# Optimization experiments

Measured on AMD Instinct MI355X. Metric: run time of the kernel, lower is better.

## Reference

```python
import jax, jax.numpy as jnp
import numpy as np

N_LAYERS = 4
EPS = 1e-5  # eqx.nn.LayerNorm default


def _kernels(lam, P, B, C, step, L):
    # Annotated-S4 DPLR generating-function kernel (Q = P), vectorized over H channels.
    # lam, P, B, C: (H, N) complex64; step: (H, 1) real. Returns K: (H, L) real.
    omega = jnp.exp((-2j * jnp.pi) * (jnp.arange(L) / L))            # (L,) roots of unity
    g = (2.0 / step) * ((1.0 - omega) / (1.0 + omega))[None, :]      # (H, L) bilinear warp
    c = 2.0 / (1.0 + omega)                                          # (L,)

    def cauchy(v):  # v: (H, N) -> (H, L): sum_n v_n / (g - lambda_n)
        return jnp.sum(v[:, None, :] / (g[:, :, None] - lam[:, None, :]), axis=-1)

    k00 = cauchy(jnp.conj(C) * B)
    k01 = cauchy(jnp.conj(C) * P)
    k10 = cauchy(jnp.conj(P) * B)
    k11 = cauchy(jnp.conj(P) * P)
    at_roots = c[None, :] * (k00 - k01 * (1.0 / (1.0 + k11)) * k10)  # woodbury correction
    return jnp.fft.ifft(at_roots, n=L, axis=-1).real                 # (H, L)


def _causal_conv(u, K):
    # u: (B, L, H) real input, K: (H, L) real kernel -> causal conv along L via zero-padded FFT.
    L = u.shape[1]
    Ud = jnp.fft.rfft(u, n=2 * L, axis=1)                 # (B, F, H)
    Kd = jnp.fft.rfft(K, n=2 * L, axis=-1)                # (H, F)
    return jnp.fft.irfft(Ud * Kd.T[None], n=2 * L, axis=1)[:, :L]


def _forward(x, enc_w, enc_b, dec_w, dec_b, lam_re, lam_im, p_re, p_im, b_re, b_im,
             c_re, c_im, d, log_step, norm_w, norm_b, w1, b1, w2, b2):
    L = x.shape[1]
    h = x @ enc_w.T + enc_b                               # encoder: (B, L, H)
    for i in range(N_LAYERS):
        skip = h
        mu = h.mean(-1, keepdims=True)
        var = ((h - mu) ** 2).mean(-1, keepdims=True)
        hn = (h - mu) / jnp.sqrt(var + EPS) * norm_w[i] + norm_b[i]
        K = _kernels(lam_re[i] + 1j * lam_im[i], p_re[i] + 1j * p_im[i],
                     b_re[i] + 1j * b_im[i], c_re[i] + 1j * c_im[i],
                     jnp.exp(log_step[i])[:, None], L)
        y = _causal_conv(hn, K) + hn * d[i]               # SSM conv + skip-through D term
        y = jax.nn.gelu(y)
        y = (y @ w1[i].T + b1[i]) * jax.nn.sigmoid(y @ w2[i].T + b2[i])  # gated MLP
        h = skip + y
    return h @ dec_w.T + dec_b                            # decoder: (B, L, out)


def setup_inputs() -> dict:
    key = jax.random.key(0)
    B, L, IN, OUT, H, N, NL = 8, 2048, 64, 64, 128, 64, N_LAYERS
    ks = jax.random.split(key, 12)
    rn = lambda k, s, sc: (jax.random.normal(k, s) * sc).astype(jnp.float32)
    return dict(
        x=rn(ks[0], (B, L, IN), 1.0),
        convolve=1,
        enc_w=rn(ks[1], (H, IN), 1.0 / np.sqrt(IN)), enc_b=jnp.zeros((H,), jnp.float32),
        dec_w=rn(ks[2], (OUT, H), 1.0 / np.sqrt(H)), dec_b=jnp.zeros((OUT,), jnp.float32),
        lam_re=-0.5 * jnp.ones((NL, H, N), jnp.float32),  # HiPPO/S4D-style stable poles
        lam_im=jnp.tile(jnp.float32(np.pi) * jnp.arange(N, dtype=jnp.float32), (NL, H, 1)),
        p_re=rn(ks[3], (NL, H, N), 0.5 / np.sqrt(N)), p_im=rn(ks[4], (NL, H, N), 0.5 / np.sqrt(N)),
        b_re=rn(ks[5], (NL, H, N), 1.0), b_im=rn(ks[6], (NL, H, N), 1.0),
        c_re=rn(ks[7], (NL, H, N), 1.0 / np.sqrt(N)), c_im=rn(ks[8], (NL, H, N), 1.0 / np.sqrt(N)),
        d=jnp.ones((NL, H), jnp.float32),
        log_step=(jax.random.uniform(ks[9], (NL, H)) * (np.log(0.1) - np.log(0.001))
                  + np.log(0.001)).astype(jnp.float32),
        norm_w=jnp.ones((NL, H), jnp.float32), norm_b=jnp.zeros((NL, H), jnp.float32),
        w1=rn(ks[10], (NL, H, H), 1.0 / np.sqrt(H)), b1=jnp.zeros((NL, H), jnp.float32),
        w2=rn(ks[11], (NL, H, H), 1.0 / np.sqrt(H)), b2=jnp.zeros((NL, H), jnp.float32),
    )


def reference(x, convolve, enc_w, enc_b, dec_w, dec_b, lam_re, lam_im, p_re, p_im,
              b_re, b_im, c_re, c_im, d, log_step, norm_w, norm_b, w1, b1, w2, b2):
    # convolve is static 1 (True): the FFT-convolution path of the S4 Model.
    return _forward(x, enc_w, enc_b, dec_w, dec_b, lam_re, lam_im, p_re, p_im, b_re, b_im,
                    c_re, c_im, d, log_step, norm_w, norm_b, w1, b1, w2, b2)
```

## Files before the change

kernel.cpp:

```cpp
#include <hip/hip_runtime.h>
#include <hip/hip_bf16.h>


#define Bsz 8
#define Lseq 2048
#define Hdim 128
#define Npol 64
#define NLAYERS 4

typedef __bf16 bf16x8 __attribute__((ext_vector_type(8)));
typedef float f32x16 __attribute__((ext_vector_type(16)));

__device__ __forceinline__ float fast_rcp(float x) { return __builtin_amdgcn_rcpf(x); }
__device__ __forceinline__ float fast_rsq(float x) { return __builtin_amdgcn_rsqf(x); }

__device__ __forceinline__ float2 cmulf(float2 a, float2 b) {
    return make_float2(a.x * b.x - a.y * b.y, a.x * b.y + a.y * b.x);
}
__device__ __forceinline__ float2 cmulc(float2 a, float2 b) {
    return make_float2(a.x * b.x + a.y * b.y, a.y * b.x - a.x * b.y);
}

__device__ __forceinline__ float gelu_f(float v) {
    float z = 0.7978845608028654f * (v + 0.044715f * v * v * v);
    float e = __expf(2.0f * z);
    return v - v * fast_rcp(e + 1.0f);
}

__device__ __forceinline__ int sw(int i) { return (i & ~15) | ((i ^ (i >> 4)) & 15); }

static __device__ const float W16R[8] = {1.f, 0.9238795325f, 0.7071067812f, 0.3826834324f,
                                         0.f, -0.3826834324f, -0.7071067812f, -0.9238795325f};
static __device__ const float W16I[8] = {0.f, -0.3826834324f, -0.7071067812f, -0.9238795325f,
                                         -1.f, -0.9238795325f, -0.7071067812f, -0.3826834324f};
static __device__ const int BR4[16] = {0, 8, 4, 12, 2, 10, 6, 14, 1, 9, 5, 13, 3, 11, 7, 15};
static __device__ const int BR3[8] = {0, 4, 2, 6, 1, 5, 3, 7};

__device__ __forceinline__ float2 twget(const float2* __restrict__ tw, int e) {
    float2 w = tw[e & 2047];
    if (e & 2048) { w.x = -w.x; w.y = -w.y; }
    return w;
}

template <bool INV>
__device__ __forceinline__ void fft16_dif(float2 v[16]) {
#pragma unroll
    for (int mi = 0; mi < 4; mi++) {
        const int m = 8 >> mi;
#pragma unroll
        for (int g = 0; g < 16; g += 2 * m) {
#pragma unroll
            for (int j = 0; j < m; j++) {
                float wr = W16R[j << mi];
                float wi = INV ? -W16I[j << mi] : W16I[j << mi];
                float2 a = v[g + j], b = v[g + j + m];
                float dx = a.x - b.x, dy = a.y - b.y;
                v[g + j] = make_float2(a.x + b.x, a.y + b.y);
                v[g + j + m] = make_float2(dx * wr - dy * wi, dx * wi + dy * wr);
            }
        }
    }
}

template <bool INV>
__device__ __forceinline__ void fft16_dit(float2 v[16]) {
#pragma unroll
    for (int mi = 3; mi >= 0; mi--) {
        const int m = 8 >> mi;
#pragma unroll
        for (int g = 0; g < 16; g += 2 * m) {
#pragma unroll
            for (int j = 0; j < m; j++) {
                float wr = W16R[j << mi];
                float wi = INV ? -W16I[j << mi] : W16I[j << mi];
                float2 a = v[g + j], b = v[g + j + m];
                float bx = b.x * wr - b.y * wi, by = b.x * wi + b.y * wr;
                v[g + j] = make_float2(a.x + bx, a.y + by);
                v[g + j + m] = make_float2(a.x - bx, a.y - by);
            }
        }
    }
}

template <bool INV>
__device__ __forceinline__ void fft8_dif(float2 v[8]) {
#pragma unroll
    for (int mi = 0; mi < 3; mi++) {
        const int m = 4 >> mi;
#pragma unroll
        for (int g = 0; g < 8; g += 2 * m) {
#pragma unroll
            for (int j = 0; j < m; j++) {
                float wr = W16R[j << (mi + 1)];
                float wi = INV ? -W16I[j << (mi + 1)] : W16I[j << (mi + 1)];
                float2 a = v[g + j], b = v[g + j + m];
                float dx = a.x - b.x, dy = a.y - b.y;
                v[g + j] = make_float2(a.x + b.x, a.y + b.y);
                v[g + j + m] = make_float2(dx * wr - dy * wi, dx * wi + dy * wr);
            }
        }
    }
}

__device__ __forceinline__ void fft4096_passA_hz(float2* data, const float2* __restrict__ tw,
                                                 int t, const float2 vin[8]) {
    float2 v[16];
#pragma unroll
    for (int j = 0; j < 8; j++) v[j] = vin[j];
#pragma unroll
    for (int j = 0; j < 8; j++)
        v[j + 8] = cmulf(v[j], make_float2(W16R[j], W16I[j]));
#pragma unroll
    for (int mi = 1; mi < 4; mi++) {
        const int m = 8 >> mi;
#pragma unroll
        for (int g = 0; g < 16; g += 2 * m) {
#pragma unroll
            for (int j = 0; j < m; j++) {
                float wr = W16R[j << mi], wi = W16I[j << mi];
                float2 a = v[g + j], b = v[g + j + m];
                float dx = a.x - b.x, dy = a.y - b.y;
                v[g + j] = make_float2(a.x + b.x, a.y + b.y);
                v[g + j + m] = make_float2(dx * wr - dy * wi, dx * wi + dy * wr);
            }
        }
    }
#pragma unroll
    for (int i = 1; i < 16; i++) v[i] = cmulf(v[i], twget(tw, t * BR4[i]));
#pragma unroll
    for (int i = 0; i < 16; i++) data[sw(i * 256 + t)] = v[i];
}

__device__ __forceinline__ void fft4096_fwd_BC(float2* data, const float2* __restrict__ tw, int t) {
    __syncthreads();
    {
        int j0 = t & 15;
        int base = (t >> 4) * 256 + j0;
        float2 v[16];
#pragma unroll
        for (int k = 0; k < 16; k++) v[k] = data[sw(base + 16 * k)];
        fft16_dif<false>(v);
#pragma unroll
        for (int i = 1; i < 16; i++) v[i] = cmulf(v[i], twget(tw, 16 * j0 * BR4[i]));
#pragma unroll
        for (int i = 0; i < 16; i++) data[sw(base + 16 * i)] = v[i];
    }
    __syncthreads();
    {
        float2 v[16];
#pragma unroll
        for (int k = 0; k < 16; k++) v[k] = data[sw(t * 16 + k)];
        fft16_dif<false>(v);
#pragma unroll
        for (int i = 0; i < 16; i++) data[sw(t * 16 + i)] = v[i];
    }
    __syncthreads();
}

__global__ __launch_bounds__(256, 4) void prep_kernel(const float* __restrict__ lam_re,
                                                      const float* __restrict__ lam_im,
                                                      const float* __restrict__ p_re,
                                                      const float* __restrict__ p_im,
                                                      const float* __restrict__ b_re,
                                                      const float* __restrict__ b_im,
                                                      const float* __restrict__ c_re,
                                                      const float* __restrict__ c_im,
                                                      const float* __restrict__ log_step,
                                                      const float* __restrict__ w1,
                                                      const float* __restrict__ w2,
                                                      float2* __restrict__ tw,
                                                      __bf16* __restrict__ wbf,
                                                      float2* __restrict__ at_roots) {
    int bid = blockIdx.x, t = threadIdx.x;
    if (bid < 8) {
        int k = bid * 256 + t;
        if (k < 2048) {
            double a = -6.283185307179586476925286766559 * (double)k / 4096.0;
            tw[k] = make_float2((float)cos(a), (float)sin(a));
        }
        return;
    }
    if (bid < 264) {
        int i = (bid - 8) * 256 + t;
        int layer = i >> 14, rem = i & 16383;
        wbf[((size_t)layer * 2) * 16384 + rem] = (__bf16)w1[i];
        wbf[((size_t)layer * 2 + 1) * 16384 + rem] = (__bf16)w2[i];
        return;
    }
    int s = bid - 264;
    int h = s & 127, layer = (s >> 7) & 3;
    int l0 = 512 * (s >> 9);
    __shared__ __align__(16) float4 polA[Npol];
    __shared__ __align__(16) float4 polB[Npol];
    __shared__ float n11S[Npol];
    int baseP = (layer * Hdim + h) * Npol;
    if (t < Npol) {
        int n = t;
        float lr = lam_re[baseP + n], li = lam_im[baseP + n];
        float pr = p_re[baseP + n], pi = p_im[baseP + n];
        float br = b_re[baseP + n], bi = b_im[baseP + n];
        float cr = c_re[baseP + n], ci = c_im[baseP + n];
        polA[n] = make_float4(lr, li, cr * br + ci * bi, cr * bi - ci * br);
        polB[n] = make_float4(cr * pr + ci * pi, cr * pi - ci * pr,
                              pr * br + pi * bi, pr * bi - pi * br);
        n11S[n] = pr * pr + pi * pi;
    }
    __syncthreads();
    float step = expf(log_step[layer * Hdim + h]);
    float gs = 2.0f / step;

    float gr[2], gi[2];
#pragma unroll
    for (int j = 0; j < 2; j++) {
        int l = l0 + t + 256 * j;
        float ang = -6.283185307179586f * (float)l / (float)Lseq;
        float wr = cosf(ang), wi = sinf(ang);
        float dr = 1.0f + wr, di = wi;
        float invd2 = fast_rcp(dr * dr + di * di);
        float nr = 1.0f - wr, ni = -wi;
        gr[j] = gs * (nr * dr + ni * di) * invd2;
        gi[j] = gs * (ni * dr - nr * di) * invd2;
    }
    float k00x[2] = {0, 0}, k00y[2] = {0, 0};
    float k01x[2] = {0, 0}, k01y[2] = {0, 0};
    float k10x[2] = {0, 0}, k10y[2] = {0, 0};
    float k11x[2] = {0, 0}, k11y[2] = {0, 0};
#pragma unroll 4
    for (int n = 0; n < Npol; n++) {
        float4 A = polA[n];
        float4 B = polB[n];
        float n11 = n11S[n];
#pragma unroll
        for (int j = 0; j < 2; j++) {
            float er = gr[j] - A.x, ei = gi[j] - A.y;
            float inv2 = fast_rcp(fmaf(er, er, ei * ei));
            float ir = er * inv2;
            float mi = ei * inv2;
            k00x[j] = fmaf(A.z, ir, fmaf(A.w, mi, k00x[j]));
            k00y[j] = fmaf(A.w, ir, fmaf(-A.z, mi, k00y[j]));
            k01x[j] = fmaf(B.x, ir, fmaf(B.y, mi, k01x[j]));
            k01y[j] = fmaf(B.y, ir, fmaf(-B.x, mi, k01y[j]));
            k10x[j] = fmaf(B.z, ir, fmaf(B.w, mi, k10x[j]));
            k10y[j] = fmaf(B.w, ir, fmaf(-B.z, mi, k10y[j]));
            k11x[j] = fmaf(n11, ir, k11x[j]);
            k11y[j] = fmaf(-n11, mi, k11y[j]);
        }
    }
#pragma unroll
    for (int j = 0; j < 2; j++) {
        int l = l0 + t + 256 * j;
        float ang = -6.283185307179586f * (float)l / (float)Lseq;
        float wr = cosf(ang), wi = sinf(ang);
        float dr = 1.0f + wr, di = wi;
        float invd2 = fast_rcp(dr * dr + di * di);
        float cr2 = 2.0f * dr * invd2, ci2 = -2.0f * di * invd2;
        float wr2 = 1.0f + k11x[j], wi2 = k11y[j];
        float w2inv = fast_rcp(fmaf(wr2, wr2, wi2 * wi2));
        float vr = wr2 * w2inv, vi = -wi2 * w2inv;
        float t1x = k01x[j] * k10x[j] - k01y[j] * k10y[j];
        float t1y = k01x[j] * k10y[j] + k01y[j] * k10x[j];
        float t2x = t1x * vr - t1y * vi, t2y = t1x * vi + t1y * vr;
        float ex = k00x[j] - t2x, ey = k00y[j] - t2y;
        at_roots[((size_t)layer * Hdim + h) * Lseq + l] =
            make_float2(cr2 * ex - ci2 * ey, cr2 * ey + ci2 * ex);
    }
}

__global__ __launch_bounds__(256) void kfft_enc_kernel(const float2* __restrict__ at_roots,
                                                       float4* __restrict__ Kd2,
                                                       const float2* __restrict__ tw,
                                                       const float* __restrict__ x,
                                                       const float* __restrict__ enc_w,
                                                       const float* __restrict__ enc_b,
                                                       const float* __restrict__ nw,
                                                       const float* __restrict__ nb,
                                                       float* __restrict__ h,
                                                       float* __restrict__ hnT) {
    __shared__ __align__(16) float smem[11712];
    int bid = blockIdx.x, t = threadIdx.x;
    if (bid < 512) {
        int hh = bid & 127, layer = bid >> 7;
        float2* data = (float2*)smem;
        float* ktmp = smem + 8192;
        const float2* src = at_roots + ((size_t)layer * Hdim + hh) * Lseq;
#pragma unroll
        for (int k = 0; k < 8; k++) {
            int l = t + 256 * k;
            data[sw(l)] = src[l];
        }
        __syncthreads();
        if (t < 128) {
            float2 v[16];
#pragma unroll
            for (int k = 0; k < 16; k++) v[k] = data[sw(t + 128 * k)];
            fft16_dif<true>(v);
#pragma unroll
            for (int i = 1; i < 16; i++) v[i] = cmulc(v[i], twget(tw, 2 * t * BR4[i]));
#pragma unroll
            for (int i = 0; i < 16; i++) data[sw(i * 128 + t)] = v[i];
        }
        __syncthreads();
        if (t < 128) {
            int i2 = t >> 3, j0 = t & 7;
            int base2 = i2 * 128 + j0;
            float2 v[16];
#pragma unroll
            for (int k = 0; k < 16; k++) v[k] = data[sw(base2 + 8 * k)];
            fft16_dif<true>(v);
#pragma unroll
            for (int i = 1; i < 16; i++) v[i] = cmulc(v[i], twget(tw, 32 * j0 * BR4[i]));
#pragma unroll
            for (int i = 0; i < 16; i++) data[sw(base2 + 8 * i)] = v[i];
        }
        __syncthreads();
        {
            float2 v8[8];
#pragma unroll
            for (int k = 0; k < 8; k++) v8[k] = data[sw(t * 8 + k)];
            fft8_dif<true>(v8);
            int r = BR4[t >> 4], s = BR4[t & 15];
#pragma unroll
            for (int i = 0; i < 8; i++) {
                int l = r + 16 * s + 256 * BR3[i];
                ktmp[l] = v8[i].x * (1.0f / 2048.0f);
            }
        }
        __syncthreads();
        {
            float2 vin[8];
#pragma unroll
            for (int k = 0; k < 8; k++) vin[k] = make_float2(ktmp[t + 256 * k], 0.f);
            fft4096_passA_hz(data, tw, t, vin);
        }
        fft4096_fwd_BC(data, tw, t);
        float2* dst = (float2*)(Kd2 + ((size_t)layer * 64 + (hh >> 1)) * 4096);
        int half = hh & 1;
#pragma unroll
        for (int k = 0; k < 16; k++) {
            int p = t + 256 * k;
            dst[2 * p + half] = data[sw(p)];
        }
    } else {
        int r0 = (bid - 512) * 16;
        float* ws = smem;
        float* xst = smem + 8320;
        float* dots = smem + 9600;
        float2* mv = (float2*)(smem + 11648);
        for (int i = t; i < 128 * 64; i += 256) ws[(i >> 6) * 65 + (i & 63)] = enc_w[i];
        for (int i = t; i < 16 * 64; i += 256) {
            int r = i >> 6, k = i & 63;
            xst[k * 20 + r] = x[(size_t)(r0 + r) * 64 + k];
        }
        __syncthreads();
        int o = t & 127, half = t >> 7;
        float acc[8];
        float bo = enc_b[o];
#pragma unroll
        for (int j = 0; j < 8; j++) acc[j] = bo;
        for (int k = 0; k < 64; k++) {
            float wv = ws[o * 65 + k];
            float4 xa = *(const float4*)&xst[k * 20 + half * 8];
            float4 xb = *(const float4*)&xst[k * 20 + half * 8 + 4];
            acc[0] += wv * xa.x; acc[1] += wv * xa.y; acc[2] += wv * xa.z; acc[3] += wv * xa.w;
            acc[4] += wv * xb.x; acc[5] += wv * xb.y; acc[6] += wv * xb.z; acc[7] += wv * xb.w;
        }
#pragma unroll
        for (int j = 0; j < 8; j++) dots[(half * 8 + j) * 128 + o] = acc[j];
        __syncthreads();
        {
            int row = t >> 4, lane = t & 15;
            float s1 = 0.f, s2 = 0.f;
#pragma unroll
            for (int i = 0; i < 8; i++) {
                float v = dots[row * 128 + lane * 8 + i];
                s1 += v; s2 += v * v;
            }
#pragma unroll
            for (int m = 1; m < 16; m <<= 1) { s1 += __shfl_xor(s1, m); s2 += __shfl_xor(s2, m); }
            if (lane == 0) {
                float mu = s1 * (1.0f / 128.0f);
                float var = s2 * (1.0f / 128.0f) - mu * mu;
                mv[row] = make_float2(mu, fast_rsq(var + 1e-5f));
            }
        }
        __syncthreads();
        int c = t & 127;
        int bb = r0 >> 11, l0 = r0 & 2047;
        float nwc = nw[c], nbc = nb[c];
        float hnv[8];
#pragma unroll
        for (int j = 0; j < 8; j++) {
            int r = half * 8 + j;
            float v = dots[r * 128 + c];
            h[(size_t)(r0 + r) * Hdim + c] = v;
            float2 m = mv[r];
            hnv[j] = (v - m.x) * m.y * nwc + nbc;
        }
        float* dst = hnT + ((size_t)bb * Hdim + c) * Lseq + l0 + half * 8;
        *(float4*)dst = make_float4(hnv[0], hnv[1], hnv[2], hnv[3]);
        *(float4*)(dst + 4) = make_float4(hnv[4], hnv[5], hnv[6], hnv[7]);
    }
}

__global__ __launch_bounds__(256) void conv_kernel(float* __restrict__ hnT,
                                                   const float4* __restrict__ Kd2,
                                                   const float* __restrict__ dvec,
                                                   const float2* __restrict__ tw) {
    int hp = blockIdx.x, b = blockIdx.y, h0 = hp * 2, t = threadIdx.x;
    __shared__ float2 data[4096];
    float* u0 = hnT + ((size_t)b * Hdim + h0) * Lseq;
    float* u1 = u0 + Lseq;
    float2 ureg[8];
    {
        float2 vin[8];
#pragma unroll
        for (int k = 0; k < 8; k++) {
            int l = t + 256 * k;
            float2 u2 = make_float2(u0[l], u1[l]);
            ureg[k] = u2;
            vin[k] = u2;
        }
        fft4096_passA_hz(data, tw, t, vin);
    }
    fft4096_fwd_BC(data, tw, t);
    const float4* Kp = Kd2 + (size_t)hp * 4096;
    const float scale = 1.0f / 4096.0f;
#pragma unroll
    for (int k = 0; k < 8; k++) {
        int p = 2 * (t + 256 * k);
        int f = __brev((unsigned)p) >> 20;
        int fm = (4096 - f) & 4095;
        int pm = __brev((unsigned)fm) >> 20;
        float2 Zf = data[sw(p)], Zm = data[sw(pm)];
        float2 U0 = make_float2(0.5f * (Zf.x + Zm.x), 0.5f * (Zf.y - Zm.y));
        float2 Dm = make_float2(Zf.x - Zm.x, Zf.y + Zm.y);
        float2 U1 = make_float2(0.5f * Dm.y, -0.5f * Dm.x);
        float4 Ka = Kp[p];
        float2 S0 = cmulf(U0, make_float2(Ka.x, Ka.y));
        float2 S1 = cmulf(U1, make_float2(Ka.z, Ka.w));
        float2 Wf = make_float2((S0.x - S1.y) * scale, (S0.y + S1.x) * scale);
        float4 Kb = Kp[pm];
        float2 U0m = make_float2(U0.x, -U0.y);
        float2 U1m = make_float2(U1.x, -U1.y);
        float2 S0m = cmulf(U0m, make_float2(Kb.x, Kb.y));
        float2 S1m = cmulf(U1m, make_float2(Kb.z, Kb.w));
        float2 Wm = make_float2((S0m.x - S1m.y) * scale, (S0m.y + S1m.x) * scale);
        data[sw(p)] = Wf;
        if (pm != p) data[sw(pm)] = Wm;
    }
    if (t == 0) {
        float2 Zf = data[sw(1)];
        float2 U0 = make_float2(Zf.x, 0.f);
        float2 U1 = make_float2(Zf.y, 0.f);
        float4 Ka = Kp[1];
        float2 S0 = cmulf(U0, make_float2(Ka.x, Ka.y));
        float2 S1 = cmulf(U1, make_float2(Ka.z, Ka.w));
        data[sw(1)] = make_float2((S0.x - S1.y) * scale, (S0.y + S1.x) * scale);
    }
    __syncthreads();
    {
        float2 v[16];
#pragma unroll
        for (int i = 0; i < 16; i++) v[i] = data[sw(t * 16 + i)];
        fft16_dit<true>(v);
#pragma unroll
        for (int i = 0; i < 16; i++) data[sw(t * 16 + i)] = v[i];
    }
    __syncthreads();
    {
        int j0 = t & 15;
        int base2 = (t >> 4) * 256 + j0;
        float2 v[16];
        v[0] = data[sw(base2)];
#pragma unroll
        for (int i = 1; i < 16; i++)
            v[i] = cmulc(data[sw(base2 + 16 * i)], twget(tw, 16 * j0 * BR4[i]));
        fft16_dit<true>(v);
#pragma unroll
        for (int i = 0; i < 16; i++) data[sw(base2 + 16 * i)] = v[i];
    }
    __syncthreads();
    {
        float2 v[16];
        v[0] = data[sw(t)];
#pragma unroll
        for (int i = 1; i < 16; i++)
            v[i] = cmulc(data[sw(i * 256 + t)], twget(tw, t * BR4[i]));
#pragma unroll
        for (int mi = 3; mi >= 1; mi--) {
            const int m = 8 >> mi;
#pragma unroll
            for (int g = 0; g < 16; g += 2 * m) {
#pragma unroll
                for (int j = 0; j < m; j++) {
                    float wr = W16R[j << mi], wi = -W16I[j << mi];
                    float2 a = v[g + j], bb2 = v[g + j + m];
                    float bx = bb2.x * wr - bb2.y * wi, by = bb2.x * wi + bb2.y * wr;
                    v[g + j] = make_float2(a.x + bx, a.y + by);
                    v[g + j + m] = make_float2(a.x - bx, a.y - by);
                }
            }
        }
#pragma unroll
        for (int j = 0; j < 8; j++) {
            float wr = W16R[j], wi = -W16I[j];
            float2 bb2 = v[j + 8];
            float bx = bb2.x * wr - bb2.y * wi, by = bb2.x * wi + bb2.y * wr;
            v[j] = make_float2(v[j].x + bx, v[j].y + by);
        }
        float d0 = dvec[h0], d1 = dvec[h0 + 1];
#pragma unroll
        for (int k = 0; k < 8; k++) {
            int l = t + 256 * k;
            u0[l] = gelu_f(v[k].x + ureg[k].x * d0);
            u1[l] = gelu_f(v[k].y + ureg[k].y * d1);
        }
    }
}

__global__ __launch_bounds__(256) void mlp_kernel(const float* __restrict__ yT,
                                                  float* __restrict__ h,
                                                  float* __restrict__ hnT,
                                                  const __bf16* __restrict__ w1b,
                                                  const __bf16* __restrict__ w2b,
                                                  const float* __restrict__ b1,
                                                  const float* __restrict__ b2,
                                                  const float* __restrict__ nw,
                                                  const float* __restrict__ nb,
                                                  int do_ln) {
    int r0 = blockIdx.x * 32;
    int t = threadIdx.x;
    int wave = t >> 6, lane = t & 63;
    __shared__ __align__(16) __bf16 ybf[32 * 136];
    __shared__ float dots[32 * 132];
    __shared__ float2 mv[32];
    int bb = r0 >> 11, l0 = r0 & 2047;
    for (int i = t; i < 32 * 128; i += 256) {
        int r = i & 31, k = i >> 5;
        ybf[r * 136 + k] = (__bf16)yT[((size_t)bb * Hdim + k) * Lseq + l0 + r];
    }
    __syncthreads();
    int m = lane & 31, half = lane >> 5;
    bf16x8 a[8];
#pragma unroll
    for (int kk = 0; kk < 8; kk++)
        a[kk] = *(const bf16x8*)&ybf[m * 136 + kk * 16 + half * 8];
    int out = 32 * wave + m;
    const __bf16* w1r = w1b + (size_t)out * 128 + half * 8;
    const __bf16* w2r = w2b + (size_t)out * 128 + half * 8;
    f32x16 acc1, acc2;
#pragma unroll
    for (int i = 0; i < 16; i++) { acc1[i] = 0.f; acc2[i] = 0.f; }
#pragma unroll
    for (int kk = 0; kk < 8; kk++) {
        bf16x8 bw1 = *(const bf16x8*)(w1r + kk * 16);
        bf16x8 bw2 = *(const bf16x8*)(w2r + kk * 16);
        acc1 = __builtin_amdgcn_mfma_f32_32x32x16_bf16(a[kk], bw1, acc1, 0, 0, 0);
        acc2 = __builtin_amdgcn_mfma_f32_32x32x16_bf16(a[kk], bw2, acc2, 0, 0, 0);
    }
    float bias1 = b1[out], bias2 = b2[out];
#pragma unroll
    for (int reg = 0; reg < 16; reg++) {
        int row = (reg & 3) + 8 * (reg >> 2) + 4 * half;
        float v1 = acc1[reg] + bias1;
        float v2 = acc2[reg] + bias2;
        float g = fast_rcp(1.0f + __expf(-v2));
        float hv = h[(size_t)(r0 + row) * Hdim + out] + v1 * g;
        dots[row * 132 + out] = hv;
    }
    __syncthreads();
    if (do_ln) {
        int row = t >> 3, lane8 = t & 7;
        float s1 = 0.f, s2 = 0.f;
        int base = row * 132 + lane8 * 16;
#pragma unroll
        for (int q = 0; q < 4; q++) {
            float4 v4 = *(const float4*)&dots[base + 4 * q];
            s1 += v4.x + v4.y + v4.z + v4.w;
            s2 += v4.x * v4.x + v4.y * v4.y + v4.z * v4.z + v4.w * v4.w;
        }
#pragma unroll
        for (int mm = 1; mm < 8; mm <<= 1) { s1 += __shfl_xor(s1, mm); s2 += __shfl_xor(s2, mm); }
        if (lane8 == 0) {
            float mu = s1 * (1.0f / 128.0f);
            float var = s2 * (1.0f / 128.0f) - mu * mu;
            mv[row] = make_float2(mu, fast_rsq(var + 1e-5f));
        }
        __syncthreads();
        int o = t & 127, rh = t >> 7;
        float nwc = nw[o], nbc = nb[o];
        float hnv[16];
#pragma unroll
        for (int j = 0; j < 16; j++) {
            int r = rh * 16 + j;
            float hvv = dots[r * 132 + o];
            h[(size_t)(r0 + r) * Hdim + o] = hvv;
            float2 mvv = mv[r];
            hnv[j] = (hvv - mvv.x) * mvv.y * nwc + nbc;
        }
        float* dst = hnT + ((size_t)bb * Hdim + o) * Lseq + l0 + rh * 16;
        *(float4*)(dst)      = make_float4(hnv[0],  hnv[1],  hnv[2],  hnv[3]);
        *(float4*)(dst + 4)  = make_float4(hnv[4],  hnv[5],  hnv[6],  hnv[7]);
        *(float4*)(dst + 8)  = make_float4(hnv[8],  hnv[9],  hnv[10], hnv[11]);
        *(float4*)(dst + 12) = make_float4(hnv[12], hnv[13], hnv[14], hnv[15]);
    } else {
        int o = t & 127, rh = t >> 7;
#pragma unroll
        for (int j = 0; j < 16; j++) {
            int r = rh * 16 + j;
            h[(size_t)(r0 + r) * Hdim + o] = dots[r * 132 + o];
        }
    }
}

__global__ __launch_bounds__(256) void decoder_kernel(const float* __restrict__ h,
                                                      const float* __restrict__ w,
                                                      const float* __restrict__ b,
                                                      float* __restrict__ out) {
    int r0 = blockIdx.x * 32;
    int t = threadIdx.x;
    __shared__ float ws[64 * 129];
    __shared__ __align__(16) float hst[128 * 36];
    for (int i = t; i < 64 * 128; i += 256) ws[(i >> 7) * 129 + (i & 127)] = w[i];
    for (int i = t; i < 32 * 128; i += 256) {
        int r = i >> 7, k = i & 127;
        hst[k * 36 + r] = h[(size_t)(r0 + r) * Hdim + k];
    }
    __syncthreads();
    int o = t & 63, q = t >> 6;
    float acc[8];
    float bo = b[o];
#pragma unroll
    for (int j = 0; j < 8; j++) acc[j] = bo;
    for (int k = 0; k < 128; k++) {
        float wv = ws[o * 129 + k];
        float4 ha = *(const float4*)&hst[k * 36 + q * 8];
        float4 hb = *(const float4*)&hst[k * 36 + q * 8 + 4];
        acc[0] += wv * ha.x; acc[1] += wv * ha.y; acc[2] += wv * ha.z; acc[3] += wv * ha.w;
        acc[4] += wv * hb.x; acc[5] += wv * hb.y; acc[6] += wv * hb.z; acc[7] += wv * hb.w;
    }
#pragma unroll
    for (int j = 0; j < 8; j++) out[(size_t)(r0 + q * 8 + j) * 64 + o] = acc[j];
}

extern "C" void kernel_launch(void* const* d_in, const int* in_sizes, int n_in,
                              void* d_out, int out_size, void* d_ws, size_t ws_size,
                              hipStream_t stream) {
    const float* x      = (const float*)d_in[0];
    const float* enc_w  = (const float*)d_in[2];
    const float* enc_b  = (const float*)d_in[3];
    const float* dec_w  = (const float*)d_in[4];
    const float* dec_b  = (const float*)d_in[5];
    const float* lam_re = (const float*)d_in[6];
    const float* lam_im = (const float*)d_in[7];
    const float* p_re   = (const float*)d_in[8];
    const float* p_im   = (const float*)d_in[9];
    const float* b_re   = (const float*)d_in[10];
    const float* b_im   = (const float*)d_in[11];
    const float* c_re   = (const float*)d_in[12];
    const float* c_im   = (const float*)d_in[13];
    const float* dvec   = (const float*)d_in[14];
    const float* lstep  = (const float*)d_in[15];
    const float* norm_w = (const float*)d_in[16];
    const float* norm_b = (const float*)d_in[17];
    const float* w1     = (const float*)d_in[18];
    const float* b1     = (const float*)d_in[19];
    const float* w2     = (const float*)d_in[20];
    const float* b2     = (const float*)d_in[21];
    float* out = (float*)d_out;

    char* ws = (char*)d_ws;
    float2* tw  = (float2*)ws;  ws += 2048 * sizeof(float2);
    float*  h   = (float*)ws;   ws += (size_t)Bsz * Lseq * Hdim * sizeof(float);
    float*  hnT = (float*)ws;   ws += (size_t)Bsz * Lseq * Hdim * sizeof(float);
    float2* atr = (float2*)ws;  ws += (size_t)NLAYERS * Hdim * Lseq * sizeof(float2);
    float4* Kd2 = (float4*)ws;  ws += (size_t)NLAYERS * (Hdim / 2) * 4096 * sizeof(float4);
    __bf16* wbf = (__bf16*)ws;  ws += (size_t)NLAYERS * 2 * Hdim * Hdim * sizeof(__bf16);

    const int nrows = Bsz * Lseq;

    prep_kernel<<<8 + 256 + 2048, 256, 0, stream>>>(
        lam_re, lam_im, p_re, p_im, b_re, b_im, c_re, c_im, lstep, w1, w2, tw, wbf, atr);
    kfft_enc_kernel<<<512 + nrows / 16, 256, 0, stream>>>(
        atr, Kd2, tw, x, enc_w, enc_b, norm_w, norm_b, h, hnT);
    for (int L = 0; L < NLAYERS; L++) {
        conv_kernel<<<dim3(Hdim / 2, Bsz), 256, 0, stream>>>(
            hnT, Kd2 + (size_t)L * (Hdim / 2) * 4096, dvec + L * Hdim, tw);
        int do_ln = (L < NLAYERS - 1) ? 1 : 0;
        const float* nwn = norm_w + ((L + 1) % NLAYERS) * Hdim;
        const float* nbn = norm_b + ((L + 1) % NLAYERS) * Hdim;
        const __bf16* w1bL = wbf + (size_t)L * 2 * Hdim * Hdim;
        const __bf16* w2bL = w1bL + Hdim * Hdim;
        mlp_kernel<<<nrows / 32, 256, 0, stream>>>(hnT, h, hnT, w1bL, w2bL,
                                                   b1 + L * Hdim, b2 + L * Hdim,
                                                   nwn, nbn, do_ln);
    }
    decoder_kernel<<<nrows / 32, 256, 0, stream>>>(h, dec_w, dec_b, out);
}
```

Measured before the change: 311.7 us.

## Replace two-channel 4096 complex FFT conv with per-channel packed real 2048 FFT

After: 320.1 us. 1.03x slower.

```diff
diff --git a/kernel.cpp b/kernel.cpp
--- a/kernel.cpp
+++ b/kernel.cpp
@@ -28,6 +28,7 @@
 }
 
 __device__ __forceinline__ int sw(int i) { return (i & ~15) | ((i ^ (i >> 4)) & 15); }
+__device__ __forceinline__ int ph(int i) { return i + (i >> 4); }
 
 static __device__ const float W16R[8] = {1.f, 0.9238795325f, 0.7071067812f, 0.3826834324f,
                                          0.f, -0.3826834324f, -0.7071067812f, -0.9238795325f};
@@ -63,26 +64,6 @@
 }
 
 template <bool INV>
-__device__ __forceinline__ void fft16_dit(float2 v[16]) {
-#pragma unroll
-    for (int mi = 3; mi >= 0; mi--) {
-        const int m = 8 >> mi;
-#pragma unroll
-        for (int g = 0; g < 16; g += 2 * m) {
-#pragma unroll
-            for (int j = 0; j < m; j++) {
-                float wr = W16R[j << mi];
-                float wi = INV ? -W16I[j << mi] : W16I[j << mi];
-                float2 a = v[g + j], b = v[g + j + m];
-                float bx = b.x * wr - b.y * wi, by = b.x * wi + b.y * wr;
-                v[g + j] = make_float2(a.x + bx, a.y + by);
-                v[g + j + m] = make_float2(a.x - bx, a.y - by);
-            }
-        }
-    }
-}
-
-template <bool INV>
 __device__ __forceinline__ void fft8_dif(float2 v[8]) {
 #pragma unroll
     for (int mi = 0; mi < 3; mi++) {
@@ -100,6 +81,50 @@
             }
         }
     }
+}
+
+template <bool INV>
+__device__ __forceinline__ void fft8_dit(float2 v[8]) {
+#pragma unroll
+    for (int mi = 2; mi >= 0; mi--) {
+        const int m = 4 >> mi;
+#pragma unroll
+        for (int g = 0; g < 8; g += 2 * m) {
+#pragma unroll
+            for (int j = 0; j < m; j++) {
+                float wr = W16R[j << (mi + 1)];
+                float wi = INV ? -W16I[j << (mi + 1)] : W16I[j << (mi + 1)];
+                float2 a = v[g + j], b = v[g + j + m];
+                float bx = b.x * wr - b.y * wi, by = b.x * wi + b.y * wr;
+                v[g + j] = make_float2(a.x + bx, a.y + by);
+                v[g + j + m] = make_float2(a.x - bx, a.y - by);
+            }
+        }
+    }
+}
+
+__device__ __forceinline__ void fft4_dif(float2 v[4]) {
+    float2 u0 = make_float2(v[0].x + v[2].x, v[0].y + v[2].y);
+    float2 u2 = make_float2(v[0].x - v[2].x, v[0].y - v[2].y);
+    float2 u1 = make_float2(v[1].x + v[3].x, v[1].y + v[3].y);
+    float2 d3 = make_float2(v[1].x - v[3].x, v[1].y - v[3].y);
+    float2 u3 = make_float2(d3.y, -d3.x);
+    v[0] = make_float2(u0.x + u1.x, u0.y + u1.y);
+    v[1] = make_float2(u0.x - u1.x, u0.y - u1.y);
+    v[2] = make_float2(u2.x + u3.x, u2.y + u3.y);
+    v[3] = make_float2(u2.x - u3.x, u2.y - u3.y);
+}
+
+__device__ __forceinline__ void fft4_dit(float2 v[4]) {
+    float2 u0 = make_float2(v[0].x + v[1].x, v[0].y + v[1].y);
+    float2 u1 = make_float2(v[0].x - v[1].x, v[0].y - v[1].y);
+    float2 u2 = make_float2(v[2].x + v[3].x, v[2].y + v[3].y);
+    float2 u3 = make_float2(v[2].x - v[3].x, v[2].y - v[3].y);
+    float2 b = make_float2(-u3.y, u3.x);
+    v[0] = make_float2(u0.x + u2.x, u0.y + u2.y);
+    v[2] = make_float2(u0.x - u2.x, u0.y - u2.y);
+    v[1] = make_float2(u1.x + b.x, u1.y + b.y);
+    v[3] = make_float2(u1.x - b.x, u1.y - b.y);
 }
 
 __device__ __forceinline__ void fft4096_passA_hz(float2* data, const float2* __restrict__ tw,
@@ -267,7 +292,7 @@
 }
 
 __global__ __launch_bounds__(256) void kfft_enc_kernel(const float2* __restrict__ at_roots,
-                                                       float4* __restrict__ Kd2,
+                                                       float4* __restrict__ Kd4,
                                                        const float2* __restrict__ tw,
                                                        const float* __restrict__ x,
                                                        const float* __restrict__ enc_w,
@@ -333,12 +358,18 @@
             fft4096_passA_hz(data, tw, t, vin);
         }
         fft4096_fwd_BC(data, tw, t);
-        float2* dst = (float2*)(Kd2 + ((size_t)layer * 64 + (hh >> 1)) * 4096);
-        int half = hh & 1;
-#pragma unroll
-        for (int k = 0; k < 16; k++) {
-            int p = t + 256 * k;
-            dst[2 * p + half] = data[sw(p)];
+        float4* dst = Kd4 + ((size_t)layer * Hdim + hh) * 2048;
+#pragma unroll
+        for (int k = 0; k < 4; k++) {
+            int pe = 2 * (t + 256 * k);
+            float2 a = data[sw(2 * pe)], bb = data[sw(2 * pe + 1)];
+            dst[pe] = make_float4(a.x, a.y, bb.x, bb.y);
+            int f = __brev((unsigned)pe) >> 21;
+            int g = (2048 - f) & 2047;
+            int pm = __brev((unsigned)g) >> 21;
+            int srcp = (pe == 0) ? 1 : pm;
+            float2 c = data[sw(2 * srcp)], d = data[sw(2 * srcp + 1)];
+            dst[pe + 1] = make_float4(c.x, c.y, d.x, d.y);
         }
     } else {
         int r0 = (bid - 512) * 16;
@@ -403,117 +434,211 @@
 }
 
 __global__ __launch_bounds__(256) void conv_kernel(float* __restrict__ hnT,
-                                                   const float4* __restrict__ Kd2,
+                                                   const float4* __restrict__ Kd4,
                                                    const float* __restrict__ dvec,
                                                    const float2* __restrict__ tw) {
-    int hp = blockIdx.x, b = blockIdx.y, h0 = hp * 2, t = threadIdx.x;
-    __shared__ float2 data[4096];
-    float* u0 = hnT + ((size_t)b * Hdim + h0) * Lseq;
-    float* u1 = u0 + Lseq;
-    float2 ureg[8];
-    {
-        float2 vin[8];
-#pragma unroll
-        for (int k = 0; k < 8; k++) {
-            int l = t + 256 * k;
-            float2 u2 = make_float2(u0[l], u1[l]);
-            ureg[k] = u2;
-            vin[k] = u2;
-        }
-        fft4096_passA_hz(data, tw, t, vin);
-    }
-    fft4096_fwd_BC(data, tw, t);
-    const float4* Kp = Kd2 + (size_t)hp * 4096;
-    const float scale = 1.0f / 4096.0f;
-#pragma unroll
-    for (int k = 0; k < 8; k++) {
-        int p = 2 * (t + 256 * k);
-        int f = __brev((unsigned)p) >> 20;
-        int fm = (4096 - f) & 4095;
-        int pm = __brev((unsigned)fm) >> 20;
-        float2 Zf = data[sw(p)], Zm = data[sw(pm)];
-        float2 U0 = make_float2(0.5f * (Zf.x + Zm.x), 0.5f * (Zf.y - Zm.y));
-        float2 Dm = make_float2(Zf.x - Zm.x, Zf.y + Zm.y);
-        float2 U1 = make_float2(0.5f * Dm.y, -0.5f * Dm.x);
-        float4 Ka = Kp[p];
-        float2 S0 = cmulf(U0, make_float2(Ka.x, Ka.y));
-        float2 S1 = cmulf(U1, make_float2(Ka.z, Ka.w));
-        float2 Wf = make_float2((S0.x - S1.y) * scale, (S0.y + S1.x) * scale);
-        float4 Kb = Kp[pm];
-        float2 U0m = make_float2(U0.x, -U0.y);
-        float2 U1m = make_float2(U1.x, -U1.y);
-        float2 S0m = cmulf(U0m, make_float2(Kb.x, Kb.y));
-        float2 S1m = cmulf(U1m, make_float2(Kb.z, Kb.w));
-        float2 Wm = make_float2((S0m.x - S1m.y) * scale, (S0m.y + S1m.x) * scale);
-        data[sw(p)] = Wf;
-        if (pm != p) data[sw(pm)] = Wm;
+    int h = blockIdx.x, b = blockIdx.y, t = threadIdx.x;
+    __shared__ float2 data[2176];
+    float* u0 = hnT + ((size_t)b * Hdim + h) * Lseq;
+    float2 zreg[4];
+    {
+        float2 v[8];
+#pragma unroll
+        for (int k = 0; k < 4; k++) {
+            int n = t + 256 * k;
+            v[k] = *(const float2*)(u0 + 2 * n);
+            zreg[k] = v[k];
+        }
+#pragma unroll
+        for (int j = 0; j < 4; j++)
+            v[j + 4] = cmulf(v[j], make_float2(W16R[2 * j], W16I[2 * j]));
+#pragma unroll
+        for (int mi = 1; mi < 3; mi++) {
+            const int m = 4 >> mi;
+#pragma unroll
+            for (int g = 0; g < 8; g += 2 * m) {
+#pragma unroll
+                for (int j = 0; j < m; j++) {
+                    float wr = W16R[j << (mi + 1)], wi = W16I[j << (mi + 1)];
+                    float2 a = v[g + j], bb = v[g + j + m];
+                    float dx = a.x - bb.x, dy = a.y - bb.y;
+                    v[g + j] = make_float2(a.x + bb.x, a.y + bb.y);
+                    v[g + j + m] = make_float2(dx * wr - dy * wi, dx * wi + dy * wr);
+                }
+            }
+        }
+#pragma unroll
+        for (int i = 1; i < 8; i++) v[i] = cmulf(v[i], twget(tw, 2 * t * BR3[i]));
+#pragma unroll
+        for (int i = 0; i < 8; i++) data[ph(t + 256 * i)] = v[i];
+    }
+    __syncthreads();
+    {
+        int j = t & 31;
+        int base = (t >> 5) * 256 + j;
+        float2 v[8];
+#pragma unroll
+        for (int i = 0; i < 8; i++) v[i] = data[ph(base + 32 * i)];
+        fft8_dif<false>(v);
+#pragma unroll
+        for (int i = 1; i < 8; i++) v[i] = cmulf(v[i], twget(tw, 16 * j * BR3[i]));
+#pragma unroll
+        for (int i = 0; i < 8; i++) data[ph(base + 32 * i)] = v[i];
+    }
+    __syncthreads();
+    {
+        int j = t & 3;
+        int base = (t >> 2) * 32 + j;
+        float2 v[8];
+#pragma unroll
+        for (int i = 0; i < 8; i++) v[i] = data[ph(base + 4 * i)];
+        fft8_dif<false>(v);
+#pragma unroll
+        for (int i = 1; i < 8; i++) v[i] = cmulf(v[i], twget(tw, 128 * j * BR3[i]));
+#pragma unroll
+        for (int i = 0; i < 8; i++) data[ph(base + 4 * i)] = v[i];
+    }
+    __syncthreads();
+    {
+#pragma unroll
+        for (int g = 0; g < 2; g++) {
+            int base = 8 * t + 4 * g;
+            float2 v[4];
+#pragma unroll
+            for (int i = 0; i < 4; i++) v[i] = data[ph(base + i)];
+            fft4_dif(v);
+#pragma unroll
+            for (int i = 0; i < 4; i++) data[ph(base + i)] = v[i];
+        }
+    }
+    __syncthreads();
+    const float4* Kp = Kd4 + (size_t)h * 2048;
+    const float hs = 0.5f / 2048.0f;
+    float dcoef = dvec[h];
+#pragma unroll
+    for (int k = 0; k < 4; k++) {
+        int idx = t + 256 * k;
+        int p = 2 * idx;
+        int f = __brev((unsigned)p) >> 21;
+        int g = (2048 - f) & 2047;
+        int pm = __brev((unsigned)g) >> 21;
+        float2 Zf = data[ph(p)], Zg = data[ph(pm)];
+        float2 W = tw[f];
+        float2 Eu = make_float2(0.5f * (Zf.x + Zg.x), 0.5f * (Zf.y - Zg.y));
+        float2 Ou = make_float2(0.5f * (Zf.y + Zg.y), -0.5f * (Zf.x - Zg.x));
+        float2 T = cmulf(W, Ou);
+        float2 Uf  = make_float2(Eu.x + T.x, Eu.y + T.y);
+        float2 Uf2 = make_float2(Eu.x - T.x, Eu.y - T.y);
+        float4 Kf = Kp[p];
+        float2 Xf  = cmulf(Uf,  make_float2(Kf.x, Kf.y));
+        float2 Xf2 = cmulf(Uf2, make_float2(Kf.z, Kf.w));
+        float2 Ep = make_float2((Xf.x + Xf2.x) * hs, (Xf.y + Xf2.y) * hs);
+        float2 Dp = make_float2((Xf.x - Xf2.x) * hs, (Xf.y - Xf2.y) * hs);
+        float2 Op = cmulc(Dp, W);
+        data[ph(p)] = make_float2(Ep.x - Op.y, Ep.y + Op.x);
+        if (pm != p) {
+            float2 Ug  = make_float2(Uf2.x, -Uf2.y);
+            float2 Ug2 = make_float2(Uf.x,  -Uf.y);
+            float4 Kg = Kp[p + 1];
+            float2 Xg  = cmulf(Ug,  make_float2(Kg.x, Kg.y));
+            float2 Xg2 = cmulf(Ug2, make_float2(Kg.z, Kg.w));
+            float2 Eg = make_float2((Xg.x + Xg2.x) * hs, (Xg.y + Xg2.y) * hs);
+            float2 Dg = make_float2((Xg.x - Xg2.x) * hs, (Xg.y - Xg2.y) * hs);
+            float2 Og = cmulf(W, Dg);
+            Og = make_float2(-Og.x, -Og.y);
+            data[ph(pm)] = make_float2(Eg.x - Og.y, Eg.y + Og.x);
+        }
     }
     if (t == 0) {
-        float2 Zf = data[sw(1)];
-        float2 U0 = make_float2(Zf.x, 0.f);
-        float2 U1 = make_float2(Zf.y, 0.f);
-        float4 Ka = Kp[1];
-        float2 S0 = cmulf(U0, make_float2(Ka.x, Ka.y));
-        float2 S1 = cmulf(U1, make_float2(Ka.z, Ka.w));
-        data[sw(1)] = make_float2((S0.x - S1.y) * scale, (S0.y + S1.x) * scale);
-    }
-    __syncthreads();
-    {
-        float2 v[16];
-#pragma unroll
-        for (int i = 0; i < 16; i++) v[i] = data[sw(t * 16 + i)];
-        fft16_dit<true>(v);
-#pragma unroll
-        for (int i = 0; i < 16; i++) data[sw(t * 16 + i)] = v[i];
-    }
-    __syncthreads();
-    {
-        int j0 = t & 15;
-        int base2 = (t >> 4) * 256 + j0;
-        float2 v[16];
-        v[0] = data[sw(base2)];
-#pragma unroll
-        for (int i = 1; i < 16; i++)
-            v[i] = cmulc(data[sw(base2 + 16 * i)], twget(tw, 16 * j0 * BR4[i]));
-        fft16_dit<true>(v);
-#pragma unroll
-        for (int i = 0; i < 16; i++) data[sw(base2 + 16 * i)] = v[i];
-    }
-    __syncthreads();
-    {
-        float2 v[16];
-        v[0] = data[sw(t)];
-#pragma unroll
-        for (int i = 1; i < 16; i++)
-            v[i] = cmulc(data[sw(i * 256 + t)], twget(tw, t * BR4[i]));
-#pragma unroll
-        for (int mi = 3; mi >= 1; mi--) {
-            const int m = 8 >> mi;
-#pragma unroll
-            for (int g = 0; g < 16; g += 2 * m) {
+        float2 Z = data[ph(1)];
+        float2 W = make_float2(0.f, -1.f);
+        float2 Eu = make_float2(Z.x, 0.f);
+        float2 Ou = make_float2(Z.y, 0.f);
+        float2 T = cmulf(W, Ou);
+        float2 Uf = make_float2(Eu.x + T.x, Eu.y + T.y);
+        float2 Uf2 = make_float2(Eu.x - T.x, Eu.y - T.y);
+        float4 Kf = Kp[1];
+        float2 Xf = cmulf(Uf, make_float2(Kf.x, Kf.y));
+        float2 Xf2 = cmulf(Uf2, make_float2(Kf.z, Kf.w));
+        float2 Ep = make_float2((Xf.x + Xf2.x) * hs, (Xf.y + Xf2.y) * hs);
+        float2 Dp = make_float2((Xf.x - Xf2.x) * hs, (Xf.y - Xf2.y) * hs);
+        float2 Op = cmulc(Dp, W);
+        data[ph(1)] = make_float2(Ep.x - Op.y, Ep.y + Op.x);
+    }
+    __syncthreads();
+    {
+#pragma unroll
+        for (int g = 0; g < 2; g++) {
+            int base = 8 * t + 4 * g;
+            float2 v[4];
+#pragma unroll
+            for (int i = 0; i < 4; i++) v[i] = data[ph(base + i)];
+            fft4_dit(v);
+#pragma unroll
+            for (int i = 0; i < 4; i++) data[ph(base + i)] = v[i];
+        }
+    }
+    __syncthreads();
+    {
+        int j = t & 3;
+        int base = (t >> 2) * 32 + j;
+        float2 v[8];
+        v[0] = data[ph(base)];
+#pragma unroll
+        for (int i = 1; i < 8; i++)
+            v[i] = cmulc(data[ph(base + 4 * i)], twget(tw, 128 * j * BR3[i]));
+        fft8_dit<true>(v);
+#pragma unroll
+        for (int i = 0; i < 8; i++) data[ph(base + 4 * i)] = v[i];
+    }
+    __syncthreads();
+    {
+        int j = t & 31;
+        int base = (t >> 5) * 256 + j;
+        float2 v[8];
+        v[0] = data[ph(base)];
+#pragma unroll
+        for (int i = 1; i < 8; i++)
+            v[i] = cmulc(data[ph(base + 32 * i)], twget(tw, 16 * j * BR3[i]));
+        fft8_dit<true>(v);
+#pragma unroll
+        for (int i = 0; i < 8; i++) data[ph(base + 32 * i)] = v[i];
+    }
+    __syncthreads();
+    {
+        float2 v[8];
+        v[0] = data[ph(t)];
+#pragma unroll
+        for (int i = 1; i < 8; i++)
+            v[i] = cmulc(data[ph(t + 256 * i)], twget(tw, 2 * t * BR3[i]));
+#pragma unroll
+        for (int mi = 2; mi >= 1; mi--) {
+            const int m = 4 >> mi;
+#pragma unroll
+            for (int g = 0; g < 8; g += 2 * m) {
 #pragma unroll
                 for (int j = 0; j < m; j++) {
-                    float wr = W16R[j << mi], wi = -W16I[j << mi];
-                    float2 a = v[g + j], bb2 = v[g + j + m];
-                    float bx = bb2.x * wr - bb2.y * wi, by = bb2.x * wi + bb2.y * wr;
+                    float wr = W16R[j << (mi + 1)], wi = -W16I[j << (mi + 1)];
+                    float2 a = v[g + j], bb = v[g + j + m];
+                    float bx = bb.x * wr - bb.y * wi, by = bb.x * wi + bb.y * wr;
                     v[g + j] = make_float2(a.x + bx, a.y + by);
                     v[g + j + m] = make_float2(a.x - bx, a.y - by);
                 }
             }
         }
 #pragma unroll
-        for (int j = 0; j < 8; j++) {
-            float wr = W16R[j], wi = -W16I[j];
-            float2 bb2 = v[j + 8];
-            float bx = bb2.x * wr - bb2.y * wi, by = bb2.x * wi + bb2.y * wr;
+        for (int j = 0; j < 4; j++) {
+            float wr = W16R[2 * j], wi = -W16I[2 * j];
+            float2 bb = v[j + 4];
+            float bx = bb.x * wr - bb.y * wi, by = bb.x * wi + bb.y * wr;
             v[j] = make_float2(v[j].x + bx, v[j].y + by);
         }
-        float d0 = dvec[h0], d1 = dvec[h0 + 1];
-#pragma unroll
-        for (int k = 0; k < 8; k++) {
-            int l = t + 256 * k;
-            u0[l] = gelu_f(v[k].x + ureg[k].x * d0);
-            u1[l] = gelu_f(v[k].y + ureg[k].y * d1);
+#pragma unroll
+        for (int k = 0; k < 4; k++) {
+            int n = t + 256 * k;
+            float y0 = gelu_f(v[k].x + zreg[k].x * dcoef);
+            float y1 = gelu_f(v[k].y + zreg[k].y * dcoef);
+            *(float2*)(u0 + 2 * n) = make_float2(y0, y1);
         }
     }
 }
@@ -674,7 +799,7 @@
     float*  h   = (float*)ws;   ws += (size_t)Bsz * Lseq * Hdim * sizeof(float);
     float*  hnT = (float*)ws;   ws += (size_t)Bsz * Lseq * Hdim * sizeof(float);
     float2* atr = (float2*)ws;  ws += (size_t)NLAYERS * Hdim * Lseq * sizeof(float2);
-    float4* Kd2 = (float4*)ws;  ws += (size_t)NLAYERS * (Hdim / 2) * 4096 * sizeof(float4);
+    float4* Kd4 = (float4*)ws;  ws += (size_t)NLAYERS * Hdim * 2048 * sizeof(float4);
     __bf16* wbf = (__bf16*)ws;  ws += (size_t)NLAYERS * 2 * Hdim * Hdim * sizeof(__bf16);
 
     const int nrows = Bsz * Lseq;
@@ -682,10 +807,10 @@
     prep_kernel<<<8 + 256 + 2048, 256, 0, stream>>>(
         lam_re, lam_im, p_re, p_im, b_re, b_im, c_re, c_im, lstep, w1, w2, tw, wbf, atr);
     kfft_enc_kernel<<<512 + nrows / 16, 256, 0, stream>>>(
-        atr, Kd2, tw, x, enc_w, enc_b, norm_w, norm_b, h, hnT);
+        atr, Kd4, tw, x, enc_w, enc_b, norm_w, norm_b, h, hnT);
     for (int L = 0; L < NLAYERS; L++) {
-        conv_kernel<<<dim3(Hdim / 2, Bsz), 256, 0, stream>>>(
-            hnT, Kd2 + (size_t)L * (Hdim / 2) * 4096, dvec + L * Hdim, tw);
+        conv_kernel<<<dim3(Hdim, Bsz), 256, 0, stream>>>(
+            hnT, Kd4 + (size_t)L * Hdim * 2048, dvec + L * Hdim, tw);
         int do_ln = (L < NLAYERS - 1) ? 1 : 0;
         const float* nwn = norm_w + ((L + 1) % NLAYERS) * Hdim;
         const float* nbn = norm_b + ((L + 1) % NLAYERS) * Hdim;
```
